# Optimization experiments

Hardware: AMD Instinct MI355X
Metric: run time of the kernel (lower is better)

The kernel has to match this reference:

```python
import jax, jax.numpy as jnp
import numpy as np

B, S, D, H = 4, 2048, 1024, 16
HD = D // H  # head_dim = 64


def setup_inputs() -> dict:
    key = jax.random.key(0)
    ks = jax.random.split(key, 9)
    sd = 1.0 / np.sqrt(D)
    x = jax.random.normal(ks[0], (B, S, D), dtype=jnp.float32)
    Wq = jax.random.normal(ks[1], (D, D), dtype=jnp.float32) * sd
    Wk = jax.random.normal(ks[2], (D, D), dtype=jnp.float32) * sd
    Wv = jax.random.normal(ks[3], (D, D), dtype=jnp.float32) * sd
    Wo = jax.random.normal(ks[4], (D, D), dtype=jnp.float32) * sd
    bq = jax.random.normal(ks[5], (D,), dtype=jnp.float32) * sd
    bk = jax.random.normal(ks[6], (D,), dtype=jnp.float32) * sd
    bv = jax.random.normal(ks[7], (D,), dtype=jnp.float32) * sd
    bo = jax.random.normal(ks[8], (D,), dtype=jnp.float32) * sd
    return {"x": x, "Wq": Wq, "bq": bq, "Wk": Wk, "bk": bk,
            "Wv": Wv, "bv": bv, "Wo": Wo, "bo": bo}


def reference(x, Wq, bq, Wk, bk, Wv, bv, Wo, bo):
    b, s, d = x.shape
    scale = jnp.float32(np.sqrt(HD))
    # projections, split into heads: (b, h, s, hd)
    def heads(y):
        return y.reshape(b, s, H, HD).transpose(0, 2, 1, 3)
    Q = heads(x @ Wq + bq)
    K = heads(x @ Wk + bk)
    V = heads(x @ Wv + bv)
    # (b, h, s, s) scores with causal mask
    scores = jnp.einsum('bhqd,bhkd->bhqk', Q, K) / scale
    causal = jnp.tril(jnp.ones((s, s), dtype=bool))
    scores = jnp.where(causal[None, None], scores, jnp.float32(-jnp.inf))
    probs = jax.nn.softmax(scores, axis=-1)
    out = jnp.einsum('bhqk,bhkd->bhqd', probs, V)
    out = out.transpose(0, 2, 1, 3).reshape(b, s, d)
    return out @ Wo + bo
```

## Files before the change

kernel.cpp:

```cpp
#include <hip/hip_runtime.h>
#include <hip/hip_bf16.h>
#include <cstdint>

typedef __bf16 bf16x8 __attribute__((ext_vector_type(8)));
typedef float f32x4 __attribute__((ext_vector_type(4)));
typedef float f32x16 __attribute__((ext_vector_type(16)));
typedef unsigned short u16t;

__device__ __forceinline__ u16t f2bf(float f) {
    uint32_t u = __builtin_bit_cast(uint32_t, f);
    u += 0x7FFF + ((u >> 16) & 1);
    return (u16t)(u >> 16);
}
__device__ __forceinline__ float bf2f(u16t v) {
    uint32_t u = (uint32_t)v << 16;
    return __builtin_bit_cast(float, u);
}

constexpr int Bb = 4, Ss = 2048, Dd = 1024, Hh = 16;
constexpr int Mrows = Bb * Ss;
constexpr float NEG = -1e30f;
constexpr float QSCALE = 0.125f * 1.44269504088896340736f;

__global__ __launch_bounds__(256) void cvt_bf16(const float* __restrict__ in,
                                                u16t* __restrict__ out, int n) {
    int i = (blockIdx.x * 256 + threadIdx.x) * 4;
    if (i >= n) return;
    float4 v = *(const float4*)(in + i);
    u16t o[4] = {f2bf(v.x), f2bf(v.y), f2bf(v.z), f2bf(v.w)};
    *(ushort4*)(out + i) = *(ushort4*)o;
}

__global__ __launch_bounds__(256) void transpose_cvt4(const float* __restrict__ W0,
                                                      const float* __restrict__ W1,
                                                      const float* __restrict__ W2,
                                                      const float* __restrict__ W3,
                                                      u16t* __restrict__ Tqkv,
                                                      u16t* __restrict__ To) {
    __shared__ float tile[64][65];
    int z = blockIdx.z;
    const float* W = z == 0 ? W0 : z == 1 ? W1 : z == 2 ? W2 : W3;
    u16t* WT = z < 3 ? Tqkv + (size_t)z * Dd * Dd : To;
    int n0 = blockIdx.x * 64, k0 = blockIdx.y * 64;
    int c = threadIdx.x & 63, r0 = (threadIdx.x >> 6) * 16;
    for (int i = 0; i < 16; i++)
        tile[c][r0 + i] = W[(size_t)(k0 + r0 + i) * Dd + n0 + c];
    __syncthreads();
    for (int i = 0; i < 16; i++)
        WT[(size_t)(n0 + r0 + i) * Dd + k0 + c] = f2bf(tile[r0 + i][c]);
}

__global__ __launch_bounds__(256) void gemm_qkv(const u16t* __restrict__ A,
                                                const u16t* __restrict__ BT,
                                                const float* __restrict__ bq,
                                                const float* __restrict__ bk,
                                                const float* __restrict__ bvv,
                                                u16t* __restrict__ Qh,
                                                u16t* __restrict__ Kh,
                                                u16t* __restrict__ Vt) {
    __shared__ __align__(16) u16t Asm[128 * 32];
    __shared__ __align__(16) u16t Bsm[128 * 32];
    int tid = threadIdx.x, lane = tid & 63, w = tid >> 6;
    int wm = w >> 1, wn = w & 1;
    int ln = lane & 15, g = lane >> 4;
    int bid = blockIdx.x;
    int wg = (bid & 7) * 192 + (bid >> 3);
    int n0 = (wg % 24) * 128, m0 = (wg / 24) * 128;

    f32x4 acc[4][4] = {};

    int sr = w * 32 + (lane >> 2);
    int sc = (((lane & 3) ^ (sr & 3)) * 8);
    const u16t* Ag0 = A + (size_t)(m0 + sr) * Dd + sc;
    const u16t* Ag1 = A + (size_t)(m0 + sr + 16) * Dd + sc;
    const u16t* Bg0 = BT + (size_t)(n0 + sr) * Dd + sc;
    const u16t* Bg1 = BT + (size_t)(n0 + sr + 16) * Dd + sc;
    u16t* As0 = &Asm[(w * 32) * 32];
    u16t* As1 = &Asm[(w * 32 + 16) * 32];
    u16t* Bs0 = &Bsm[(w * 32) * 32];
    u16t* Bs1 = &Bsm[(w * 32 + 16) * 32];

    for (int k0 = 0; k0 < Dd; k0 += 32) {
        __syncthreads();
        __builtin_amdgcn_global_load_lds(Ag0 + k0, As0, 16, 0, 0);
        __builtin_amdgcn_global_load_lds(Ag1 + k0, As1, 16, 0, 0);
        __builtin_amdgcn_global_load_lds(Bg0 + k0, Bs0, 16, 0, 0);
        __builtin_amdgcn_global_load_lds(Bg1 + k0, Bs1, 16, 0, 0);
        __syncthreads();
        bf16x8 af[4], bf[4];
        #pragma unroll
        for (int i = 0; i < 4; i++) {
            int row = wm * 64 + i * 16 + ln;
            af[i] = *(const bf16x8*)&Asm[row * 32 + ((g ^ (row & 3)) * 8)];
        }
        #pragma unroll
        for (int j = 0; j < 4; j++) {
            int row = wn * 64 + j * 16 + ln;
            bf[j] = *(const bf16x8*)&Bsm[row * 32 + ((g ^ (row & 3)) * 8)];
        }
        #pragma unroll
        for (int i = 0; i < 4; i++)
            #pragma unroll
            for (int j = 0; j < 4; j++)
                acc[i][j] = __builtin_amdgcn_mfma_f32_16x16x32_bf16(af[i], bf[j], acc[i][j], 0, 0, 0);
    }

    #pragma unroll
    for (int i = 0; i < 4; i++) {
        #pragma unroll
        for (int j = 0; j < 4; j++) {
            int col = n0 + wn * 64 + j * 16 + ln;
            int seg = col >> 10, c1k = col & 1023;
            float bias = seg == 0 ? bq[c1k] : seg == 1 ? bk[c1k] : bvv[c1k];
            int rowb = m0 + wm * 64 + i * 16 + g * 4;
            int b = rowb >> 11, s = rowb & 2047, h = c1k >> 6, hd = c1k & 63;
            if (seg == 0) {
                for (int r = 0; r < 4; r++) {
                    float v = (acc[i][j][r] + bias) * QSCALE;
                    Qh[((size_t)(b * Hh + h) * Ss + s + r) * 64 + hd] = f2bf(v);
                }
            } else if (seg == 1) {
                for (int r = 0; r < 4; r++)
                    Kh[((size_t)(b * Hh + h) * Ss + s + r) * 64 + hd] = f2bf(acc[i][j][r] + bias);
            } else {
                u16t pk4[4];
                for (int r = 0; r < 4; r++) pk4[r] = f2bf(acc[i][j][r] + bias);
                *(ushort4*)(Vt + ((size_t)((b * Hh + h) * 64 + hd) << 11) + s) = *(ushort4*)pk4;
            }
        }
    }
}

__global__ __launch_bounds__(256) void gemm_o(const u16t* __restrict__ A,
                                              const u16t* __restrict__ BT,
                                              const float* __restrict__ bias,
                                              float* __restrict__ outF) {
    __shared__ __align__(16) u16t Asm[128 * 32];
    __shared__ __align__(16) u16t Bsm[128 * 32];
    int tid = threadIdx.x, lane = tid & 63, w = tid >> 6;
    int wm = w >> 1, wn = w & 1;
    int ln = lane & 15, g = lane >> 4;
    int bid = blockIdx.x;
    int wg = (bid & 7) * 64 + (bid >> 3);
    int n0 = (wg & 7) * 128, m0 = (wg >> 3) * 128;

    f32x4 acc[4][4] = {};

    int sr = w * 32 + (lane >> 2);
    int sc = (((lane & 3) ^ (sr & 3)) * 8);
    const u16t* Ag0 = A + (size_t)(m0 + sr) * Dd + sc;
    const u16t* Ag1 = A + (size_t)(m0 + sr + 16) * Dd + sc;
    const u16t* Bg0 = BT + (size_t)(n0 + sr) * Dd + sc;
    const u16t* Bg1 = BT + (size_t)(n0 + sr + 16) * Dd + sc;
    u16t* As0 = &Asm[(w * 32) * 32];
    u16t* As1 = &Asm[(w * 32 + 16) * 32];
    u16t* Bs0 = &Bsm[(w * 32) * 32];
    u16t* Bs1 = &Bsm[(w * 32 + 16) * 32];

    for (int k0 = 0; k0 < Dd; k0 += 32) {
        __syncthreads();
        __builtin_amdgcn_global_load_lds(Ag0 + k0, As0, 16, 0, 0);
        __builtin_amdgcn_global_load_lds(Ag1 + k0, As1, 16, 0, 0);
        __builtin_amdgcn_global_load_lds(Bg0 + k0, Bs0, 16, 0, 0);
        __builtin_amdgcn_global_load_lds(Bg1 + k0, Bs1, 16, 0, 0);
        __syncthreads();
        bf16x8 af[4], bf[4];
        #pragma unroll
        for (int i = 0; i < 4; i++) {
            int row = wm * 64 + i * 16 + ln;
            af[i] = *(const bf16x8*)&Asm[row * 32 + ((g ^ (row & 3)) * 8)];
        }
        #pragma unroll
        for (int j = 0; j < 4; j++) {
            int row = wn * 64 + j * 16 + ln;
            bf[j] = *(const bf16x8*)&Bsm[row * 32 + ((g ^ (row & 3)) * 8)];
        }
        #pragma unroll
        for (int i = 0; i < 4; i++)
            #pragma unroll
            for (int j = 0; j < 4; j++)
                acc[i][j] = __builtin_amdgcn_mfma_f32_16x16x32_bf16(af[i], bf[j], acc[i][j], 0, 0, 0);
    }

    #pragma unroll
    for (int i = 0; i < 4; i++) {
        #pragma unroll
        for (int j = 0; j < 4; j++) {
            int col = n0 + wn * 64 + j * 16 + ln;
            float bv = bias[col];
            int rowb = m0 + wm * 64 + i * 16 + g * 4;
            for (int r = 0; r < 4; r++)
                outF[(size_t)(rowb + r) * Dd + col] = acc[i][j][r] + bv;
        }
    }
}

__global__ __launch_bounds__(256, 4) void attn(const u16t* __restrict__ Qh,
                                               const u16t* __restrict__ Kh,
                                               const u16t* __restrict__ Vt,
                                               u16t* __restrict__ Opart,
                                               float2* __restrict__ ml) {
    __shared__ __align__(16) u16t Ksm[2][64 * 64];
    __shared__ __align__(16) u16t Vsm[2][64 * 64];

    int tid = threadIdx.x, lane = tid & 63, w = tid >> 6;
    int l31 = lane & 31, hi = lane >> 5;
    int flat = blockIdx.y * 16 + blockIdx.x;
    int xcd = flat & 7, jj = flat >> 3;
    int bh = xcd * 8 + (jj >> 4);
    int i = jj & 15;

    const u16t* Kb = Kh + (size_t)bh * Ss * 64;
    const u16t* Vb = Vt + (size_t)bh * 64 * Ss;

    int sr0 = w * 16 + (lane >> 3);
    int sr1 = sr0 + 8;
    int sc0 = (((lane & 7) ^ (sr0 & 7) ^ ((sr0 >> 3) & 3)) * 8);
    int sc1 = (((lane & 7) ^ (sr1 & 7) ^ ((sr1 >> 3) & 3)) * 8);
    const u16t* Kg0 = Kb + (size_t)sr0 * 64 + sc0;
    const u16t* Kg1 = Kb + (size_t)sr1 * 64 + sc1;
    const u16t* Vg0 = Vb + (size_t)sr0 * Ss + sc0;
    const u16t* Vg1 = Vb + (size_t)sr1 * Ss + sc1;

    auto stage = [&](int buf, int t) {
        size_t koff = (size_t)t * 64 * 64;
        size_t voff = (size_t)t * 64;
        __builtin_amdgcn_global_load_lds(Kg0 + koff, &Ksm[buf][(w * 2 + 0) * 512], 16, 0, 0);
        __builtin_amdgcn_global_load_lds(Kg1 + koff, &Ksm[buf][(w * 2 + 1) * 512], 16, 0, 0);
        __builtin_amdgcn_global_load_lds(Vg0 + voff, &Vsm[buf][(w * 2 + 0) * 512], 16, 0, 0);
        __builtin_amdgcn_global_load_lds(Vg1 + voff, &Vsm[buf][(w * 2 + 1) * 512], 16, 0, 0);
    };

    int swzr = (l31 & 7) ^ ((l31 >> 3) & 3);

    for (int task = 0; task < 2; task++) {
        int qx = task == 0 ? i : 15 - i;
        int tstart = task == 0 ? 0 : qx + 1;
        int tend = task == 0 ? qx + 1 : 2 * qx + 2;
        int qb = qx * 128;
        int q0w = qb + w * 32;
        int qlane = q0w + l31;

        bf16x8 qB[4];
        {
            const u16t* Qp = Qh + ((size_t)bh * Ss + qlane) * 64 + hi * 8;
            #pragma unroll
            for (int ks = 0; ks < 4; ks++)
                qB[ks] = *(const bf16x8*)(Qp + 16 * ks);
        }

        f32x16 oacc[2] = {};
        float m_run = NEG, l_run = 0.f;

        stage(0, tstart);
        __syncthreads();

        for (int t = tstart; t < tend; t++) {
            int cur = (t - tstart) & 1;
            int kv0 = t << 6;
            if (t + 1 < tend) stage(cur ^ 1, t + 1);

            bool active = (kv0 <= q0w + 31);
            if (active) {
                f32x16 p0 = {}, p1 = {};
                __builtin_amdgcn_s_setprio(1);
                #pragma unroll
                for (int ks = 0; ks < 4; ks++) {
                    int cc = (2 * ks + hi) ^ swzr;
                    bf16x8 ka0 = *(const bf16x8*)&Ksm[cur][(size_t)l31 * 64 + cc * 8];
                    bf16x8 ka1 = *(const bf16x8*)&Ksm[cur][(size_t)(32 + l31) * 64 + cc * 8];
                    p0 = __builtin_amdgcn_mfma_f32_32x32x16_bf16(ka0, qB[ks], p0, 0, 0, 0);
                    p1 = __builtin_amdgcn_mfma_f32_32x32x16_bf16(ka1, qB[ks], p1, 0, 0, 0);
                }
                __builtin_amdgcn_s_setprio(0);

                float pv[32];
                #pragma unroll
                for (int r = 0; r < 16; r++) { pv[r] = p0[r]; pv[16 + r] = p1[r]; }

                if (kv0 + 63 > q0w) {
                    #pragma unroll
                    for (int ti = 0; ti < 2; ti++)
                        #pragma unroll
                        for (int r = 0; r < 16; r++) {
                            int kvg = kv0 + 32 * ti + (r & 3) + 8 * (r >> 2) + 4 * hi;
                            if (kvg > qlane) pv[16 * ti + r] = NEG;
                        }
                }

                float mt = fmaxf(pv[0], pv[1]);
                #pragma unroll
                for (int r = 2; r < 32; r += 2)
                    mt = fmaxf(fmaxf(mt, pv[r]), pv[r + 1]);
                mt = fmaxf(mt, __shfl_xor(mt, 32));
                if (__any(mt > m_run + 10.0f)) {
                    float mn = fmaxf(m_run, mt);
                    float al = __builtin_exp2f(m_run - mn);
                    m_run = mn;
                    l_run *= al;
                    #pragma unroll
                    for (int r = 0; r < 16; r++) { oacc[0][r] *= al; oacc[1][r] *= al; }
                }
                #pragma unroll
                for (int r = 0; r < 32; r++) pv[r] = __builtin_exp2f(pv[r] - m_run);
                float sa = 0.f, sb = 0.f, sc_ = 0.f, sd = 0.f;
                #pragma unroll
                for (int r = 0; r < 32; r += 4) {
                    sa += pv[r]; sb += pv[r + 1]; sc_ += pv[r + 2]; sd += pv[r + 3];
                }
                float rsum = (sa + sb) + (sc_ + sd);
                rsum += __shfl_xor(rsum, 32);
                l_run += rsum;

                bf16x8 pb[4];
                #pragma unroll
                for (int half = 0; half < 2; half++) {
                    const int base = 16 * half;
                    uint32_t c0, c1, c2, c3;
                    asm("v_cvt_pk_bf16_f32 %0, %1, %2" : "=v"(c0) : "v"(pv[base + 0]), "v"(pv[base + 1]));
                    asm("v_cvt_pk_bf16_f32 %0, %1, %2" : "=v"(c1) : "v"(pv[base + 2]), "v"(pv[base + 3]));
                    asm("v_cvt_pk_bf16_f32 %0, %1, %2" : "=v"(c2) : "v"(pv[base + 4]), "v"(pv[base + 5]));
                    asm("v_cvt_pk_bf16_f32 %0, %1, %2" : "=v"(c3) : "v"(pv[base + 6]), "v"(pv[base + 7]));
                    asm volatile("v_permlane32_swap_b32 %0, %1" : "+v"(c0), "+v"(c2));
                    asm volatile("v_permlane32_swap_b32 %0, %1" : "+v"(c1), "+v"(c3));
                    uint32_t w4[4] = {c0, c1, c2, c3};
                    pb[2 * half] = *(bf16x8*)w4;
                    uint32_t d0, d1, d2, d3;
                    asm("v_cvt_pk_bf16_f32 %0, %1, %2" : "=v"(d0) : "v"(pv[base + 8]),  "v"(pv[base + 9]));
                    asm("v_cvt_pk_bf16_f32 %0, %1, %2" : "=v"(d1) : "v"(pv[base + 10]), "v"(pv[base + 11]));
                    asm("v_cvt_pk_bf16_f32 %0, %1, %2" : "=v"(d2) : "v"(pv[base + 12]), "v"(pv[base + 13]));
                    asm("v_cvt_pk_bf16_f32 %0, %1, %2" : "=v"(d3) : "v"(pv[base + 14]), "v"(pv[base + 15]));
                    asm volatile("v_permlane32_swap_b32 %0, %1" : "+v"(d0), "+v"(d2));
                    asm volatile("v_permlane32_swap_b32 %0, %1" : "+v"(d1), "+v"(d3));
                    uint32_t w5[4] = {d0, d1, d2, d3};
                    pb[2 * half + 1] = *(bf16x8*)w5;
                }

                __builtin_amdgcn_s_setprio(1);
                #pragma unroll
                for (int dt = 0; dt < 2; dt++) {
                    int drow = dt * 32 + l31;
                    #pragma unroll
                    for (int ks = 0; ks < 4; ks++) {
                        int cc = (2 * ks + hi) ^ swzr;
                        bf16x8 va = *(const bf16x8*)&Vsm[cur][(size_t)drow * 64 + cc * 8];
                        oacc[dt] = __builtin_amdgcn_mfma_f32_32x32x16_bf16(va, pb[ks], oacc[dt], 0, 0, 0);
                    }
                }
                __builtin_amdgcn_s_setprio(0);
            }
            __syncthreads();
        }

        int u = (bh * 16 + qx) * 2 + task;
        int qloc = w * 32 + l31;
        if (hi == 0) {
            float2 v;
            v.x = m_run; v.y = l_run;
            ml[u * 128 + qloc] = v;
        }
        u16t* Op = Opart + ((size_t)u * 128 + qloc) * 64;
        #pragma unroll
        for (int dt = 0; dt < 2; dt++)
            #pragma unroll
            for (int rq = 0; rq < 4; rq++) {
                u16t pk4[4];
                #pragma unroll
                for (int j = 0; j < 4; j++) pk4[j] = f2bf(oacc[dt][rq * 4 + j]);
                int d0 = dt * 32 + rq * 8 + hi * 4;
                *(ushort4*)(Op + d0) = *(ushort4*)pk4;
            }
    }
}

__global__ __launch_bounds__(256) void attn_merge(const u16t* __restrict__ Opart,
                                                  const float2* __restrict__ ml,
                                                  u16t* __restrict__ Ob) {
    int r = blockIdx.x * 256 + threadIdx.x;
    int bh = r >> 11, q = r & 2047;
    int qx = q >> 7, qloc = q & 127;
    int u0 = (bh * 16 + qx) * 2, u1 = u0 + 1;
    float2 a = ml[u0 * 128 + qloc];
    float2 b = ml[u1 * 128 + qloc];
    float m = fmaxf(a.x, b.x);
    float e0 = __builtin_exp2f(a.x - m);
    float e1 = __builtin_exp2f(b.x - m);
    float inv = 1.0f / (a.y * e0 + b.y * e1);
    float f0 = e0 * inv, f1 = e1 * inv;
    const uint4* p0 = (const uint4*)(Opart + ((size_t)u0 * 128 + qloc) * 64);
    const uint4* p1 = (const uint4*)(Opart + ((size_t)u1 * 128 + qloc) * 64);
    int bb = bh >> 4, hh = bh & 15;
    u16t* dst = Ob + ((size_t)(bb * Ss + q)) * Dd + hh * 64;
    #pragma unroll
    for (int c = 0; c < 8; c++) {
        uint4 x = p0[c], y = p1[c];
        const u16t* px = (const u16t*)&x;
        const u16t* py = (const u16t*)&y;
        uint4 o;
        u16t* po = (u16t*)&o;
        #pragma unroll
        for (int k = 0; k < 8; k++)
            po[k] = f2bf(bf2f(px[k]) * f0 + bf2f(py[k]) * f1);
        *(uint4*)(dst + c * 8) = o;
    }
}

extern "C" void kernel_launch(void* const* d_in, const int* in_sizes, int n_in,
                              void* d_out, int out_size, void* d_ws, size_t ws_size,
                              hipStream_t stream) {
    const float* x  = (const float*)d_in[0];
    const float* Wq = (const float*)d_in[1];
    const float* bq = (const float*)d_in[2];
    const float* Wk = (const float*)d_in[3];
    const float* bk = (const float*)d_in[4];
    const float* Wv = (const float*)d_in[5];
    const float* bv = (const float*)d_in[6];
    const float* Wo = (const float*)d_in[7];
    const float* bo = (const float*)d_in[8];

    constexpr size_t MB = 1024 * 1024;
    char* ws = (char*)d_ws;
    size_t off = 0;
    auto alloc = [&](size_t bytes) { char* p = ws + off; off += (bytes + 255) & ~(size_t)255; return p; };

    char* R = alloc(34 * MB);
    float2* ml   = (float2*)R;
    u16t* Opart  = (u16t*)(R + 2 * MB);
    u16t* xb     = (u16t*)R;
    u16t* WqkvT  = (u16t*)(R + 16 * MB);
    u16t* WoT    = (u16t*)alloc((size_t)Dd * Dd * 2);
    u16t* Qh     = (u16t*)alloc((size_t)Mrows * Dd * 2);
    u16t* Kh     = (u16t*)alloc((size_t)Mrows * Dd * 2);
    u16t* Vtp    = (u16t*)alloc((size_t)Mrows * Dd * 2);
    u16t* Ob     = Qh;

    int nx = Mrows * Dd;
    cvt_bf16<<<nx / (256 * 4), 256, 0, stream>>>(x, xb, nx);
    dim3 tg(16, 16, 4);
    transpose_cvt4<<<tg, 256, 0, stream>>>(Wq, Wk, Wv, Wo, WqkvT, WoT);

    gemm_qkv<<<1536, 256, 0, stream>>>(xb, WqkvT, bq, bk, bv, Qh, Kh, Vtp);

    dim3 ga(16, Bb * Hh);
    attn<<<ga, 256, 0, stream>>>(Qh, Kh, Vtp, Opart, ml);
    attn_merge<<<512, 256, 0, stream>>>(Opart, ml, Ob);

    gemm_o<<<512, 256, 0, stream>>>(Ob, WoT, bo, (float*)d_out);
}
```

Before: 219.2 us.

## Triple-buffer GEMM LDS loads and compute softmax row sums via MFMA

Both projection GEMMs now use a three-stage LDS ring filled by async global_load_lds, with vmcnt-based waits and a single barrier per k-step instead of two, so loads for tile t+2 overlap the MFMAs on tile t. In the attention kernel, the row sum of probabilities is no longer reduced on the VALU with a cross-lane shuffle. It is accumulated by extra MFMAs that multiply a ones vector by the packed bf16 probabilities, which also removes the pv copy array. The GEMMs pay triple the LDS footprint, and the row sum is now taken from bf16-rounded probabilities, which slightly changes the normaliser.

Result: slower. 230.2 us (+5.0%).

```diff
diff --git a/kernel.cpp b/kernel.cpp
--- a/kernel.cpp
+++ b/kernel.cpp
@@ -58,8 +58,8 @@
                                                 u16t* __restrict__ Qh,
                                                 u16t* __restrict__ Kh,
                                                 u16t* __restrict__ Vt) {
-    __shared__ __align__(16) u16t Asm[128 * 32];
-    __shared__ __align__(16) u16t Bsm[128 * 32];
+    __shared__ __align__(16) u16t Asm[3][128 * 32];
+    __shared__ __align__(16) u16t Bsm[3][128 * 32];
     int tid = threadIdx.x, lane = tid & 63, w = tid >> 6;
     int wm = w >> 1, wn = w & 1;
     int ln = lane & 15, g = lane >> 4;
@@ -75,34 +75,45 @@
     const u16t* Ag1 = A + (size_t)(m0 + sr + 16) * Dd + sc;
     const u16t* Bg0 = BT + (size_t)(n0 + sr) * Dd + sc;
     const u16t* Bg1 = BT + (size_t)(n0 + sr + 16) * Dd + sc;
-    u16t* As0 = &Asm[(w * 32) * 32];
-    u16t* As1 = &Asm[(w * 32 + 16) * 32];
-    u16t* Bs0 = &Bsm[(w * 32) * 32];
-    u16t* Bs1 = &Bsm[(w * 32 + 16) * 32];
-
-    for (int k0 = 0; k0 < Dd; k0 += 32) {
-        __syncthreads();
-        __builtin_amdgcn_global_load_lds(Ag0 + k0, As0, 16, 0, 0);
-        __builtin_amdgcn_global_load_lds(Ag1 + k0, As1, 16, 0, 0);
-        __builtin_amdgcn_global_load_lds(Bg0 + k0, Bs0, 16, 0, 0);
-        __builtin_amdgcn_global_load_lds(Bg1 + k0, Bs1, 16, 0, 0);
-        __syncthreads();
+
+    auto stage = [&](int buf, int k0) {
+        __builtin_amdgcn_global_load_lds(Ag0 + k0, &Asm[buf][(w * 32) * 32], 16, 0, 0);
+        __builtin_amdgcn_global_load_lds(Ag1 + k0, &Asm[buf][(w * 32 + 16) * 32], 16, 0, 0);
+        __builtin_amdgcn_global_load_lds(Bg0 + k0, &Bsm[buf][(w * 32) * 32], 16, 0, 0);
+        __builtin_amdgcn_global_load_lds(Bg1 + k0, &Bsm[buf][(w * 32 + 16) * 32], 16, 0, 0);
+    };
+
+    stage(0, 0);
+    stage(1, 32);
+    asm volatile("s_waitcnt vmcnt(4)" ::: "memory");
+    __builtin_amdgcn_sched_barrier(0);
+    __builtin_amdgcn_s_barrier();
+
+    for (int t = 0; t < 32; t++) {
+        int cur = t % 3;
+        if (t < 30) stage((t + 2) % 3, (t + 2) * 32);
         bf16x8 af[4], bf[4];
         #pragma unroll
         for (int i = 0; i < 4; i++) {
             int row = wm * 64 + i * 16 + ln;
-            af[i] = *(const bf16x8*)&Asm[row * 32 + ((g ^ (row & 3)) * 8)];
+            af[i] = *(const bf16x8*)&Asm[cur][row * 32 + ((g ^ (row & 3)) * 8)];
         }
         #pragma unroll
         for (int j = 0; j < 4; j++) {
             int row = wn * 64 + j * 16 + ln;
-            bf[j] = *(const bf16x8*)&Bsm[row * 32 + ((g ^ (row & 3)) * 8)];
-        }
+            bf[j] = *(const bf16x8*)&Bsm[cur][row * 32 + ((g ^ (row & 3)) * 8)];
+        }
+        __builtin_amdgcn_s_setprio(1);
         #pragma unroll
         for (int i = 0; i < 4; i++)
             #pragma unroll
             for (int j = 0; j < 4; j++)
                 acc[i][j] = __builtin_amdgcn_mfma_f32_16x16x32_bf16(af[i], bf[j], acc[i][j], 0, 0, 0);
+        __builtin_amdgcn_s_setprio(0);
+        if (t < 30) asm volatile("s_waitcnt vmcnt(4)" ::: "memory");
+        else        asm volatile("s_waitcnt vmcnt(0)" ::: "memory");
+        __builtin_amdgcn_sched_barrier(0);
+        __builtin_amdgcn_s_barrier();
     }
 
     #pragma unroll
@@ -135,8 +146,8 @@
                                               const u16t* __restrict__ BT,
                                               const float* __restrict__ bias,
                                               float* __restrict__ outF) {
-    __shared__ __align__(16) u16t Asm[128 * 32];
-    __shared__ __align__(16) u16t Bsm[128 * 32];
+    __shared__ __align__(16) u16t Asm[3][128 * 32];
+    __shared__ __align__(16) u16t Bsm[3][128 * 32];
     int tid = threadIdx.x, lane = tid & 63, w = tid >> 6;
     int wm = w >> 1, wn = w & 1;
     int ln = lane & 15, g = lane >> 4;
@@ -152,34 +163,45 @@
     const u16t* Ag1 = A + (size_t)(m0 + sr + 16) * Dd + sc;
     const u16t* Bg0 = BT + (size_t)(n0 + sr) * Dd + sc;
     const u16t* Bg1 = BT + (size_t)(n0 + sr + 16) * Dd + sc;
-    u16t* As0 = &Asm[(w * 32) * 32];
-    u16t* As1 = &Asm[(w * 32 + 16) * 32];
-    u16t* Bs0 = &Bsm[(w * 32) * 32];
-    u16t* Bs1 = &Bsm[(w * 32 + 16) * 32];
-
-    for (int k0 = 0; k0 < Dd; k0 += 32) {
-        __syncthreads();
-        __builtin_amdgcn_global_load_lds(Ag0 + k0, As0, 16, 0, 0);
-        __builtin_amdgcn_global_load_lds(Ag1 + k0, As1, 16, 0, 0);
-        __builtin_amdgcn_global_load_lds(Bg0 + k0, Bs0, 16, 0, 0);
-        __builtin_amdgcn_global_load_lds(Bg1 + k0, Bs1, 16, 0, 0);
-        __syncthreads();
+
+    auto stage = [&](int buf, int k0) {
+        __builtin_amdgcn_global_load_lds(Ag0 + k0, &Asm[buf][(w * 32) * 32], 16, 0, 0);
+        __builtin_amdgcn_global_load_lds(Ag1 + k0, &Asm[buf][(w * 32 + 16) * 32], 16, 0, 0);
+        __builtin_amdgcn_global_load_lds(Bg0 + k0, &Bsm[buf][(w * 32) * 32], 16, 0, 0);
+        __builtin_amdgcn_global_load_lds(Bg1 + k0, &Bsm[buf][(w * 32 + 16) * 32], 16, 0, 0);
+    };
+
+    stage(0, 0);
+    stage(1, 32);
+    asm volatile("s_waitcnt vmcnt(4)" ::: "memory");
+    __builtin_amdgcn_sched_barrier(0);
+    __builtin_amdgcn_s_barrier();
+
+    for (int t = 0; t < 32; t++) {
+        int cur = t % 3;
+        if (t < 30) stage((t + 2) % 3, (t + 2) * 32);
         bf16x8 af[4], bf[4];
         #pragma unroll
         for (int i = 0; i < 4; i++) {
             int row = wm * 64 + i * 16 + ln;
-            af[i] = *(const bf16x8*)&Asm[row * 32 + ((g ^ (row & 3)) * 8)];
+            af[i] = *(const bf16x8*)&Asm[cur][row * 32 + ((g ^ (row & 3)) * 8)];
         }
         #pragma unroll
         for (int j = 0; j < 4; j++) {
             int row = wn * 64 + j * 16 + ln;
-            bf[j] = *(const bf16x8*)&Bsm[row * 32 + ((g ^ (row & 3)) * 8)];
-        }
+            bf[j] = *(const bf16x8*)&Bsm[cur][row * 32 + ((g ^ (row & 3)) * 8)];
+        }
+        __builtin_amdgcn_s_setprio(1);
         #pragma unroll
         for (int i = 0; i < 4; i++)
             #pragma unroll
             for (int j = 0; j < 4; j++)
                 acc[i][j] = __builtin_amdgcn_mfma_f32_16x16x32_bf16(af[i], bf[j], acc[i][j], 0, 0, 0);
+        __builtin_amdgcn_s_setprio(0);
+        if (t < 30) asm volatile("s_waitcnt vmcnt(4)" ::: "memory");
+        else        asm volatile("s_waitcnt vmcnt(0)" ::: "memory");
+        __builtin_amdgcn_sched_barrier(0);
+        __builtin_amdgcn_s_barrier();
     }
 
     #pragma unroll
@@ -232,6 +254,9 @@
     };
 
     int swzr = (l31 & 7) ^ ((l31 >> 3) & 3);
+    uint32_t one2 = 0x3F803F80u;
+    uint32_t onesw[4] = {one2, one2, one2, one2};
+    bf16x8 ones8 = *(bf16x8*)onesw;
 
     for (int task = 0; task < 2; task++) {
         int qx = task == 0 ? i : 15 - i;
@@ -250,7 +275,8 @@
         }
 
         f32x16 oacc[2] = {};
-        float m_run = NEG, l_run = 0.f;
+        f32x16 lacc = {};
+        float m_run = NEG;
 
         stage(0, tstart);
         __syncthreads();
@@ -274,66 +300,79 @@
                 }
                 __builtin_amdgcn_s_setprio(0);
 
-                float pv[32];
-                #pragma unroll
-                for (int r = 0; r < 16; r++) { pv[r] = p0[r]; pv[16 + r] = p1[r]; }
-
                 if (kv0 + 63 > q0w) {
                     #pragma unroll
-                    for (int ti = 0; ti < 2; ti++)
-                        #pragma unroll
-                        for (int r = 0; r < 16; r++) {
-                            int kvg = kv0 + 32 * ti + (r & 3) + 8 * (r >> 2) + 4 * hi;
-                            if (kvg > qlane) pv[16 * ti + r] = NEG;
-                        }
-                }
-
-                float mt = fmaxf(pv[0], pv[1]);
-                #pragma unroll
-                for (int r = 2; r < 32; r += 2)
-                    mt = fmaxf(fmaxf(mt, pv[r]), pv[r + 1]);
+                    for (int r = 0; r < 16; r++) {
+                        int kvg = kv0 + (r & 3) + 8 * (r >> 2) + 4 * hi;
+                        if (kvg > qlane) p0[r] = NEG;
+                        if (kvg + 32 > qlane) p1[r] = NEG;
+                    }
+                }
+
+                float ma = fmaxf(p0[0], p1[0]), mb = fmaxf(p0[1], p1[1]);
+                float mc = fmaxf(p0[2], p1[2]), md = fmaxf(p0[3], p1[3]);
+                #pragma unroll
+                for (int r = 4; r < 16; r += 4) {
+                    ma = fmaxf(ma, fmaxf(p0[r], p1[r]));
+                    mb = fmaxf(mb, fmaxf(p0[r + 1], p1[r + 1]));
+                    mc = fmaxf(mc, fmaxf(p0[r + 2], p1[r + 2]));
+                    md = fmaxf(md, fmaxf(p0[r + 3], p1[r + 3]));
+                }
+                float mt = fmaxf(fmaxf(ma, mb), fmaxf(mc, md));
                 mt = fmaxf(mt, __shfl_xor(mt, 32));
                 if (__any(mt > m_run + 10.0f)) {
                     float mn = fmaxf(m_run, mt);
                     float al = __builtin_exp2f(m_run - mn);
                     m_run = mn;
-                    l_run *= al;
                     #pragma unroll
-                    for (int r = 0; r < 16; r++) { oacc[0][r] *= al; oacc[1][r] *= al; }
-                }
-                #pragma unroll
-                for (int r = 0; r < 32; r++) pv[r] = __builtin_exp2f(pv[r] - m_run);
-                float sa = 0.f, sb = 0.f, sc_ = 0.f, sd = 0.f;
-                #pragma unroll
-                for (int r = 0; r < 32; r += 4) {
-                    sa += pv[r]; sb += pv[r + 1]; sc_ += pv[r + 2]; sd += pv[r + 3];
-                }
-                float rsum = (sa + sb) + (sc_ + sd);
-                rsum += __shfl_xor(rsum, 32);
-                l_run += rsum;
+                    for (int r = 0; r < 16; r++) {
+                        oacc[0][r] *= al; oacc[1][r] *= al; lacc[r] *= al;
+                    }
+                }
+                #pragma unroll
+                for (int r = 0; r < 16; r++) {
+                    p0[r] = __builtin_exp2f(p0[r] - m_run);
+                    p1[r] = __builtin_exp2f(p1[r] - m_run);
+                }
 
                 bf16x8 pb[4];
-                #pragma unroll
-                for (int half = 0; half < 2; half++) {
-                    const int base = 16 * half;
+                {
                     uint32_t c0, c1, c2, c3;
-                    asm("v_cvt_pk_bf16_f32 %0, %1, %2" : "=v"(c0) : "v"(pv[base + 0]), "v"(pv[base + 1]));
-                    asm("v_cvt_pk_bf16_f32 %0, %1, %2" : "=v"(c1) : "v"(pv[base + 2]), "v"(pv[base + 3]));
-                    asm("v_cvt_pk_bf16_f32 %0, %1, %2" : "=v"(c2) : "v"(pv[base + 4]), "v"(pv[base + 5]));
-                    asm("v_cvt_pk_bf16_f32 %0, %1, %2" : "=v"(c3) : "v"(pv[base + 6]), "v"(pv[base + 7]));
+                    asm("v_cvt_pk_bf16_f32 %0, %1, %2" : "=v"(c0) : "v"(p0[0]), "v"(p0[1]));
+                    asm("v_cvt_pk_bf16_f32 %0, %1, %2" : "=v"(c1) : "v"(p0[2]), "v"(p0[3]));
+                    asm("v_cvt_pk_bf16_f32 %0, %1, %2" : "=v"(c2) : "v"(p0[4]), "v"(p0[5]));
+                    asm("v_cvt_pk_bf16_f32 %0, %1, %2" : "=v"(c3) : "v"(p0[6]), "v"(p0[7]));
                     asm volatile("v_permlane32_swap_b32 %0, %1" : "+v"(c0), "+v"(c2));
                     asm volatile("v_permlane32_swap_b32 %0, %1" : "+v"(c1), "+v"(c3));
                     uint32_t w4[4] = {c0, c1, c2, c3};
-                    pb[2 * half] = *(bf16x8*)w4;
+                    pb[0] = *(bf16x8*)w4;
                     uint32_t d0, d1, d2, d3;
-                    asm("v_cvt_pk_bf16_f32 %0, %1, %2" : "=v"(d0) : "v"(pv[base + 8]),  "v"(pv[base + 9]));
-                    asm("v_cvt_pk_bf16_f32 %0, %1, %2" : "=v"(d1) : "v"(pv[base + 10]), "v"(pv[base + 11]));
-                    asm("v_cvt_pk_bf16_f32 %0, %1, %2" : "=v"(d2) : "v"(pv[base + 12]), "v"(pv[base + 13]));
-                    asm("v_cvt_pk_bf16_f32 %0, %1, %2" : "=v"(d3) : "v"(pv[base + 14]), "v"(pv[base + 15]));
+                    asm("v_cvt_pk_bf16_f32 %0, %1, %2" : "=v"(d0) : "v"(p0[8]),  "v"(p0[9]));
+                    asm("v_cvt_pk_bf16_f32 %0, %1, %2" : "=v"(d1) : "v"(p0[10]), "v"(p0[11]));
+                    asm("v_cvt_pk_bf16_f32 %0, %1, %2" : "=v"(d2) : "v"(p0[12]), "v"(p0[13]));
+                    asm("v_cvt_pk_bf16_f32 %0, %1, %2" : "=v"(d3) : "v"(p0[14]), "v"(p0[15]));
                     asm volatile("v_permlane32_swap_b32 %0, %1" : "+v"(d0), "+v"(d2));
                     asm volatile("v_permlane32_swap_b32 %0, %1" : "+v"(d1), "+v"(d3));
                     uint32_t w5[4] = {d0, d1, d2, d3};
-                    pb[2 * half + 1] = *(bf16x8*)w5;
+                    pb[1] = *(bf16x8*)w5;
+                    uint32_t e0, e1, e2, e3;
+                    asm("v_cvt_pk_bf16_f32 %0, %1, %2" : "=v"(e0) : "v"(p1[0]), "v"(p1[1]));
+                    asm("v_cvt_pk_bf16_f32 %0, %1, %2" : "=v"(e1) : "v"(p1[2]), "v"(p1[3]));
+                    asm("v_cvt_pk_bf16_f32 %0, %1, %2" : "=v"(e2) : "v"(p1[4]), "v"(p1[5]));
+                    asm("v_cvt_pk_bf16_f32 %0, %1, %2" : "=v"(e3) : "v"(p1[6]), "v"(p1[7]));
+                    asm volatile("v_permlane32_swap_b32 %0, %1" : "+v"(e0), "+v"(e2));
+                    asm volatile("v_permlane32_swap_b32 %0, %1" : "+v"(e1), "+v"(e3));
+                    uint32_t w6[4] = {e0, e1, e2, e3};
+                    pb[2] = *(bf16x8*)w6;
+                    uint32_t f0, f1, f2, f3;
+                    asm("v_cvt_pk_bf16_f32 %0, %1, %2" : "=v"(f0) : "v"(p1[8]),  "v"(p1[9]));
+                    asm("v_cvt_pk_bf16_f32 %0, %1, %2" : "=v"(f1) : "v"(p1[10]), "v"(p1[11]));
+                    asm("v_cvt_pk_bf16_f32 %0, %1, %2" : "=v"(f2) : "v"(p1[12]), "v"(p1[13]));
+                    asm("v_cvt_pk_bf16_f32 %0, %1, %2" : "=v"(f3) : "v"(p1[14]), "v"(p1[15]));
+                    asm volatile("v_permlane32_swap_b32 %0, %1" : "+v"(f0), "+v"(f2));
+                    asm volatile("v_permlane32_swap_b32 %0, %1" : "+v"(f1), "+v"(f3));
+                    uint32_t w7[4] = {f0, f1, f2, f3};
+                    pb[3] = *(bf16x8*)w7;
                 }
 
                 __builtin_amdgcn_s_setprio(1);
@@ -347,6 +386,9 @@
                         oacc[dt] = __builtin_amdgcn_mfma_f32_32x32x16_bf16(va, pb[ks], oacc[dt], 0, 0, 0);
                     }
                 }
+                #pragma unroll
+                for (int ks = 0; ks < 4; ks++)
+                    lacc = __builtin_amdgcn_mfma_f32_32x32x16_bf16(ones8, pb[ks], lacc, 0, 0, 0);
                 __builtin_amdgcn_s_setprio(0);
             }
             __syncthreads();
@@ -356,7 +398,7 @@
         int qloc = w * 32 + l31;
         if (hi == 0) {
             float2 v;
-            v.x = m_run; v.y = l_run;
+            v.x = m_run; v.y = lacc[0];
             ml[u * 128 + qloc] = v;
         }
         u16t* Op = Opart + ((size_t)u * 128 + qloc) * 64;
```
